# Kernel tuning notes

Hardware: AMD Instinct MI355X
Metric: run time of the kernel (lower is better)

The kernel has to match this reference:

```python
import jax, jax.numpy as jnp
import numpy as np

N, E, D = 10000, 160000, 512
H, C = 4, 128          # hidden layers: 4 heads x 128 = 512 (residual-compatible)
HF, CF = 2, 512        # final layer: 2 heads, concat=False (mean)
NEG_SLOPE = 0.2


def _gat(x, src, dst, W, a_src, a_dst, b, heads, out_c, concat):
    """PyG-style GATConv (v1 attention), no dropout (eval mode)."""
    n = x.shape[0]
    h = (x @ W).reshape(n, heads, out_c)                  # [N,H,C]
    es = (h * a_src).sum(-1)                              # [N,H]
    ed = (h * a_dst).sum(-1)                              # [N,H]
    e = jax.nn.leaky_relu(es[src] + ed[dst], NEG_SLOPE)   # [E,H]
    m = jax.ops.segment_max(e, dst, num_segments=n)       # softmax over in-edges of dst
    m = jnp.where(jnp.isfinite(m), m, 0.0)                # guard isolated nodes
    ex = jnp.exp(e - m[dst])
    den = jax.ops.segment_sum(ex, dst, num_segments=n)
    alpha = ex / (den[dst] + 1e-16)                       # [E,H]
    msg = h[src] * alpha[..., None]                       # [E,H,C]
    out = jax.ops.segment_sum(msg, dst, num_segments=n)   # [N,H,C]
    out = out.reshape(n, heads * out_c) if concat else out.mean(axis=1)
    return out + b


def setup_inputs() -> dict:
    key = jax.random.key(0)
    ks = jax.random.split(key, 16)
    s = 0.05
    return {
        "graph": jax.random.normal(ks[0], (N, D), jnp.float32),
        "edge_index": jax.random.randint(ks[1], (2, E), 0, N, dtype=jnp.int32),
        "W1": jax.random.normal(ks[2], (D, H * C), jnp.float32) * s,
        "as1": jax.random.normal(ks[3], (H, C), jnp.float32) * s,
        "ad1": jax.random.normal(ks[4], (H, C), jnp.float32) * s,
        "b1": jnp.zeros((H * C,), jnp.float32),
        "W2": jax.random.normal(ks[5], (H * C, H * C), jnp.float32) * s,
        "as2": jax.random.normal(ks[6], (H, C), jnp.float32) * s,
        "ad2": jax.random.normal(ks[7], (H, C), jnp.float32) * s,
        "b2": jnp.zeros((H * C,), jnp.float32),
        "W3": jax.random.normal(ks[8], (H * C, HF * CF), jnp.float32) * s,
        "as3": jax.random.normal(ks[9], (HF, CF), jnp.float32) * s,
        "ad3": jax.random.normal(ks[10], (HF, CF), jnp.float32) * s,
        "b3": jnp.zeros((CF,), jnp.float32),
    }


def reference(graph, edge_index, W1, as1, ad1, b1, W2, as2, ad2, b2, W3, as3, ad3, b3):
    src, dst = edge_index[0], edge_index[1]
    # layer_size=2: conv1 + convs[0] with ELU+residual, convs[1] (concat=False) residual only
    x = jax.nn.elu(_gat(graph, src, dst, W1, as1, ad1, b1, H, C, True) + graph)
    x = jax.nn.elu(_gat(x, src, dst, W2, as2, ad2, b2, H, C, True) + x)
    x = _gat(x, src, dst, W3, as3, ad3, b3, HF, CF, False) + x
    return x
```

## Files before the change

### kernel.cpp

```cpp
#include <hip/hip_runtime.h>
#include <hip/hip_bf16.h>
#include <hip/hip_fp16.h>
#include <cstddef>
#include <cstdint>


typedef _Float16 half8 __attribute__((ext_vector_type(8)));
typedef _Float16 half4v __attribute__((ext_vector_type(4)));
typedef _Float16 half2v __attribute__((ext_vector_type(2)));
typedef float floatx4 __attribute__((ext_vector_type(4)));

#define AS1(p) ((const __attribute__((address_space(1))) void*)(p))
#define AS3(p) ((__attribute__((address_space(3))) void*)(p))


__global__ void count_deg(const int* __restrict__ dst, int* __restrict__ deg, int E) {
    int e = blockIdx.x * blockDim.x + threadIdx.x;
    if (e < E) atomicAdd(&deg[dst[e]], 1);
}

__global__ void scan_kernel(const int* __restrict__ deg, int* __restrict__ row_start,
                            int* __restrict__ cursor, int n) {
    __shared__ int wsum[16];
    __shared__ int carry_s;
    int tid = threadIdx.x;
    int wave = tid >> 6, lane = tid & 63;
    if (tid == 0) { carry_s = 0; row_start[0] = 0; }
    __syncthreads();
    for (int base = 0; base < n; base += 1024) {
        int i = base + tid;
        int v = (i < n) ? deg[i] : 0;
        int x = v;
#pragma unroll
        for (int off = 1; off < 64; off <<= 1) {
            int t = __shfl_up(x, off);
            if (lane >= off) x += t;
        }
        if (lane == 63) wsum[wave] = x;
        __syncthreads();
        if (wave == 0 && lane < 16) {
            int w = wsum[lane];
#pragma unroll
            for (int off = 1; off < 16; off <<= 1) {
                int t = __shfl_up(w, off);
                if (lane >= off) w += t;
            }
            wsum[lane] = w;
        }
        __syncthreads();
        int carry = carry_s;
        int incl = x + (wave ? wsum[wave - 1] : 0) + carry;
        if (i < n) { row_start[i + 1] = incl; cursor[i] = incl - v; }
        __syncthreads();
        if (tid == 1023) carry_s = incl;
        __syncthreads();
    }
}

__global__ void scatter_edges(const int* __restrict__ src, const int* __restrict__ dst,
                              int* __restrict__ cursor, int* __restrict__ srcs, int E) {
    int e = blockIdx.x * blockDim.x + threadIdx.x;
    if (e < E) {
        int p = atomicAdd(&cursor[dst[e]], 1);
        srcs[p] = src[e];
    }
}


__global__ void cast_f16(const float* __restrict__ in, _Float16* __restrict__ out, int n4) {
    int i = blockIdx.x * blockDim.x + threadIdx.x;
    if (i < n4) {
        float4 v = ((const float4*)in)[i];
        half4v o = {(_Float16)v.x, (_Float16)v.y, (_Float16)v.z, (_Float16)v.w};
        ((half4v*)out)[i] = o;
    }
}

__global__ void transpose_cast_g(const float* __restrict__ in, _Float16* __restrict__ out,
                                 int in_ld, int out_ld) {
    __shared__ float t[32][33];
    int r0 = blockIdx.y * 32, c0 = blockIdx.x * 32;
    int tx = threadIdx.x, ty = threadIdx.y;
    for (int i = ty; i < 32; i += 8)
        t[i][tx] = in[(size_t)(r0 + i) * in_ld + c0 + tx];
    __syncthreads();
    for (int i = ty; i < 32; i += 8)
        out[(size_t)(c0 + i) * out_ld + r0 + tx] = (_Float16)t[tx][i];
}

__global__ void proj_all(const float* __restrict__ W1, const float* __restrict__ as1,
                         const float* __restrict__ ad1,
                         const float* __restrict__ W2, const float* __restrict__ as2,
                         const float* __restrict__ ad2,
                         const float* __restrict__ W3, const float* __restrict__ as3,
                         const float* __restrict__ ad3,
                         _Float16* __restrict__ Wt1, _Float16* __restrict__ Wt2,
                         float* __restrict__ wes3, float* __restrict__ wed3) {
    int w = (blockIdx.x * blockDim.x + threadIdx.x) >> 6;
    int lane = threadIdx.x & 63;
    if (w < 8192) {
        int layer = w >> 12;
        int idx = w & 4095;
        int d = idx & 511, hh = (idx >> 9) & 3, sel = idx >> 11;
        const float* W = layer ? W2 : W1;
        const float* a = layer ? (sel ? ad2 : as2) : (sel ? ad1 : as1);
        const float* row = W + (size_t)d * 512 + hh * 128;
        const float* av = a + hh * 128;
        float s = 0.f;
        s += row[lane] * av[lane];
        s += row[lane + 64] * av[lane + 64];
#pragma unroll
        for (int off = 32; off; off >>= 1) s += __shfl_down(s, off);
        if (lane == 0) {
            _Float16* Wt = layer ? Wt2 : Wt1;
            Wt[(size_t)(512 + sel * 4 + hh) * 512 + d] = (_Float16)s;
        }
    } else if (w < 10240) {
        int idx = w - 8192;
        int k = idx & 511, hh = (idx >> 9) & 1, sel = idx >> 10;
        const float* a = (sel ? ad3 : as3) + hh * 512;
        const float* row = W3 + (size_t)k * 1024 + hh * 512;
        float s = 0.f;
        for (int c = lane; c < 512; c += 64) s += row[c] * a[c];
#pragma unroll
        for (int off = 32; off; off >>= 1) s += __shfl_down(s, off);
        if (lane == 0) (sel ? wed3 : wes3)[hh * 512 + k] = s;
    } else if (w < 11136) {
        int z = (w - 10240) * 64 + lane;
        int layer = z / 28672;
        int rem = z - layer * 28672;
        int row = 520 + rem / 512, col = rem & 511;
        (layer ? Wt2 : Wt1)[(size_t)row * 512 + col] = (_Float16)0.f;
    }
}


#define BK 64

__global__ __launch_bounds__(256) void gemm_f16_att(const _Float16* __restrict__ A,
                                                    const _Float16* __restrict__ Bt,
                                                    _Float16* __restrict__ Hout,
                                                    float* __restrict__ es,
                                                    float* __restrict__ ed,
                                                    int M, int K) {
    __shared__ _Float16 As[64 * BK];
    __shared__ _Float16 Bs[64 * BK];
    int tid = threadIdx.x;
    int lane = tid & 63, wave = tid >> 6;
    int wm = (wave & 1) * 32, wn = (wave >> 1) * 32;
    int m0 = blockIdx.y * 64, n0 = blockIdx.x * 64;
    int l15 = lane & 15, quad = lane >> 4;
    int trow = tid >> 3, tcol = tid & 7;

    floatx4 acc[2][2];
#pragma unroll
    for (int i = 0; i < 2; ++i)
#pragma unroll
        for (int j = 0; j < 2; ++j) acc[i][j] = (floatx4){0.f, 0.f, 0.f, 0.f};

    for (int k0 = 0; k0 < K; k0 += BK) {
        __syncthreads();
#pragma unroll
        for (int i = 0; i < 2; ++i) {
            int gr = m0 + i * 32 + trow; if (gr >= M) gr = M - 1;
            __builtin_amdgcn_global_load_lds(AS1(A + (size_t)gr * K + k0 + tcol * 8),
                                             AS3(As + (size_t)(i * 256 + tid) * 8), 16, 0, 0);
        }
#pragma unroll
        for (int i = 0; i < 2; ++i) {
            int gr = n0 + i * 32 + trow;
            __builtin_amdgcn_global_load_lds(AS1(Bt + (size_t)gr * K + k0 + tcol * 8),
                                             AS3(Bs + (size_t)(i * 256 + tid) * 8), 16, 0, 0);
        }
        __syncthreads();
#pragma unroll
        for (int ks = 0; ks < BK; ks += 32) {
            half8 af[2], bfr[2];
#pragma unroll
            for (int i = 0; i < 2; ++i)
                af[i] = *(const half8*)&As[(wm + i * 16 + l15) * BK + ks + quad * 8];
#pragma unroll
            for (int j = 0; j < 2; ++j)
                bfr[j] = *(const half8*)&Bs[(wn + j * 16 + l15) * BK + ks + quad * 8];
#pragma unroll
            for (int i = 0; i < 2; ++i)
#pragma unroll
                for (int j = 0; j < 2; ++j)
                    acc[i][j] = __builtin_amdgcn_mfma_f32_16x16x32_f16(af[i], bfr[j], acc[i][j], 0, 0, 0);
        }
    }
#pragma unroll
    for (int i = 0; i < 2; ++i)
#pragma unroll
        for (int j = 0; j < 2; ++j) {
            int col = n0 + wn + j * 16 + l15;
#pragma unroll
            for (int r = 0; r < 4; ++r) {
                int row = m0 + wm + i * 16 + quad * 4 + r;
                if (row < M) {
                    float v = acc[i][j][r];
                    if (col < 512) Hout[(size_t)row * 512 + col] = (_Float16)v;
                    else if (col < 516) es[row * 4 + col - 512] = v;
                    else if (col < 520) ed[row * 4 + col - 516] = v;
                }
            }
        }
}

__global__ __launch_bounds__(256) void gemm_f16_ep(const _Float16* __restrict__ A,
                                                   const _Float16* __restrict__ Bt,
                                                   float* __restrict__ out,
                                                   const float* __restrict__ bias,
                                                   const _Float16* __restrict__ xres,
                                                   int M, int Nn, int K) {
    __shared__ _Float16 As[64 * BK];
    __shared__ _Float16 Bs[64 * BK];
    int tid = threadIdx.x;
    int lane = tid & 63, wave = tid >> 6;
    int wm = (wave & 1) * 32, wn = (wave >> 1) * 32;
    int m0 = blockIdx.y * 64, n0 = blockIdx.x * 64;
    int l15 = lane & 15, quad = lane >> 4;
    int trow = tid >> 3, tcol = tid & 7;

    floatx4 acc[2][2];
#pragma unroll
    for (int i = 0; i < 2; ++i)
#pragma unroll
        for (int j = 0; j < 2; ++j) acc[i][j] = (floatx4){0.f, 0.f, 0.f, 0.f};

    for (int k0 = 0; k0 < K; k0 += BK) {
        __syncthreads();
#pragma unroll
        for (int i = 0; i < 2; ++i) {
            int gr = m0 + i * 32 + trow; if (gr >= M) gr = M - 1;
            __builtin_amdgcn_global_load_lds(AS1(A + (size_t)gr * K + k0 + tcol * 8),
                                             AS3(As + (size_t)(i * 256 + tid) * 8), 16, 0, 0);
        }
#pragma unroll
        for (int i = 0; i < 2; ++i) {
            int gr = n0 + i * 32 + trow;
            __builtin_amdgcn_global_load_lds(AS1(Bt + (size_t)gr * K + k0 + tcol * 8),
                                             AS3(Bs + (size_t)(i * 256 + tid) * 8), 16, 0, 0);
        }
        __syncthreads();
#pragma unroll
        for (int ks = 0; ks < BK; ks += 32) {
            half8 af[2], bfr[2];
#pragma unroll
            for (int i = 0; i < 2; ++i)
                af[i] = *(const half8*)&As[(wm + i * 16 + l15) * BK + ks + quad * 8];
#pragma unroll
            for (int j = 0; j < 2; ++j)
                bfr[j] = *(const half8*)&Bs[(wn + j * 16 + l15) * BK + ks + quad * 8];
#pragma unroll
            for (int i = 0; i < 2; ++i)
#pragma unroll
                for (int j = 0; j < 2; ++j)
                    acc[i][j] = __builtin_amdgcn_mfma_f32_16x16x32_f16(af[i], bfr[j], acc[i][j], 0, 0, 0);
        }
    }
#pragma unroll
    for (int i = 0; i < 2; ++i)
#pragma unroll
        for (int j = 0; j < 2; ++j) {
            int col = n0 + wn + j * 16 + l15;
#pragma unroll
            for (int r = 0; r < 4; ++r) {
                int row = m0 + wm + i * 16 + quad * 4 + r;
                if (row < M)
                    out[(size_t)row * Nn + col] =
                        0.5f * acc[i][j][r] + bias[col] + (float)xres[(size_t)row * Nn + col];
            }
        }
}


template <int H>
__global__ __launch_bounds__(256) void attn_alpha2(
    const float* __restrict__ es, const float* __restrict__ ed,
    const int* __restrict__ row_start, const int* __restrict__ srcs,
    float* __restrict__ alpha, float* __restrict__ den, int Nn, int E) {
    const int EP = 64 / H;
    int wave = threadIdx.x >> 6, lane = threadIdx.x & 63;
    int n = blockIdx.x * 4 + wave;
    if (n >= Nn) return;
    int h = lane & (H - 1);
    int eslot = lane / H;
    float edn = ed[n * H + h];
    int beg = row_start[n], end = row_start[n + 1];
    float m = -INFINITY;
    for (int j0 = beg; j0 < end; j0 += EP) {
        int j = j0 + eslot;
        float e = -INFINITY;
        if (j < end) {
            e = es[srcs[j] * H + h] + edn;
            e = (e > 0.f) ? e : 0.2f * e;
            alpha[(size_t)h * E + j] = e;
        }
        m = fmaxf(m, e);
    }
#pragma unroll
    for (int off = H; off < 64; off <<= 1) m = fmaxf(m, __shfl_xor(m, off));
    float dsum = 0.f;
    for (int j0 = beg; j0 < end; j0 += EP) {
        int j = j0 + eslot;
        if (j < end) {
            float w = __expf(alpha[(size_t)h * E + j] - m);
            alpha[(size_t)h * E + j] = w;
            dsum += w;
        }
    }
#pragma unroll
    for (int off = H; off < 64; off <<= 1) dsum += __shfl_xor(dsum, off);
    if (lane < H) den[n * H + lane] = dsum;
}


template <bool RES32, bool COEF3>
__global__ __launch_bounds__(512) void aggregate4_concat(
    const _Float16* __restrict__ h, const float* __restrict__ alpha,
    const float* __restrict__ den,
    const int* __restrict__ row_start, const int* __restrict__ srcs,
    const float* __restrict__ bias, const float* __restrict__ xres32,
    const _Float16* __restrict__ xres16, _Float16* __restrict__ x_out_h,
    const float* __restrict__ wes3, const float* __restrict__ wed3,
    float* __restrict__ es3, float* __restrict__ ed3, int E) {
    __shared__ float red[8][512];
    __shared__ float csum[8][4];
    int n = blockIdx.x;
    int tid = threadIdx.x;
    int slot = tid >> 6, lane = tid & 63;
    int head = lane >> 4;
    int c0 = lane * 8;
    const float* al = alpha + (size_t)head * E;
    int beg = row_start[n], end = row_start[n + 1];
    float acc[8] = {};
    int j = beg + slot;
    for (; j + 8 < end; j += 16) {
        int s0 = srcs[j], s1 = srcs[j + 8];
        float w0 = al[j], w1 = al[j + 8];
        half8 h0 = *(const half8*)&h[(size_t)s0 * 512 + c0];
        half8 h1 = *(const half8*)&h[(size_t)s1 * 512 + c0];
#pragma unroll
        for (int k = 0; k < 8; ++k) acc[k] += w0 * (float)h0[k];
#pragma unroll
        for (int k = 0; k < 8; ++k) acc[k] += w1 * (float)h1[k];
    }
    if (j < end) {
        int s = srcs[j];
        float w = al[j];
        half8 hv = *(const half8*)&h[(size_t)s * 512 + c0];
#pragma unroll
        for (int k = 0; k < 8; ++k) acc[k] += w * (float)hv[k];
    }
#pragma unroll
    for (int k = 0; k < 8; ++k) red[slot][c0 + k] = acc[k];
    __syncthreads();
    int c = tid;
    float invden = 1.f / (den[n * 4 + (c >> 7)] + 1e-16f);
    float s = red[0][c] + red[1][c] + red[2][c] + red[3][c] +
              red[4][c] + red[5][c] + red[6][c] + red[7][c];
    size_t base = (size_t)n * 512 + c;
    float res = RES32 ? xres32[base] : (float)xres16[base];
    float v = s * invden + bias[c] + res;
    v = (v > 0.f) ? v : expm1f(v);
    x_out_h[base] = (_Float16)v;
    if (COEF3) {
        float t0 = v * wes3[c], t1 = v * wes3[512 + c];
        float t2 = v * wed3[c], t3 = v * wed3[512 + c];
#pragma unroll
        for (int off = 32; off; off >>= 1) {
            t0 += __shfl_down(t0, off);
            t1 += __shfl_down(t1, off);
            t2 += __shfl_down(t2, off);
            t3 += __shfl_down(t3, off);
        }
        if (lane == 0) {
            csum[slot][0] = t0; csum[slot][1] = t1;
            csum[slot][2] = t2; csum[slot][3] = t3;
        }
        __syncthreads();
        if (tid == 0) {
            float a0 = 0, a1 = 0, a2 = 0, a3 = 0;
#pragma unroll
            for (int w = 0; w < 8; ++w) {
                a0 += csum[w][0]; a1 += csum[w][1];
                a2 += csum[w][2]; a3 += csum[w][3];
            }
            es3[n * 2] = a0; es3[n * 2 + 1] = a1;
            ed3[n * 2] = a2; ed3[n * 2 + 1] = a3;
        }
    }
}


__global__ __launch_bounds__(512) void aggregate_x_dual(
    const _Float16* __restrict__ x, const float* __restrict__ alpha,
    const float* __restrict__ den,
    const int* __restrict__ row_start, const int* __restrict__ srcs,
    _Float16* __restrict__ y, int E) {
    __shared__ float red[8][1024];
    int n = blockIdx.x;
    int tid = threadIdx.x;
    int slot = tid >> 6, lane = tid & 63;
    int c0 = lane * 8;
    const float* al0 = alpha;
    const float* al1 = alpha + E;
    int beg = row_start[n], end = row_start[n + 1];
    float a0[8] = {}, a1[8] = {};
    int j = beg + slot;
    for (; j + 8 < end; j += 16) {
        int s0 = srcs[j], s1 = srcs[j + 8];
        float u0 = al0[j], v0 = al1[j];
        float u1 = al0[j + 8], v1 = al1[j + 8];
        half8 h0 = *(const half8*)&x[(size_t)s0 * 512 + c0];
        half8 h1 = *(const half8*)&x[(size_t)s1 * 512 + c0];
#pragma unroll
        for (int k = 0; k < 8; ++k) {
            float f = (float)h0[k];
            a0[k] += u0 * f;
            a1[k] += v0 * f;
        }
#pragma unroll
        for (int k = 0; k < 8; ++k) {
            float f = (float)h1[k];
            a0[k] += u1 * f;
            a1[k] += v1 * f;
        }
    }
    if (j < end) {
        int s = srcs[j];
        float u = al0[j], v = al1[j];
        half8 hv = *(const half8*)&x[(size_t)s * 512 + c0];
#pragma unroll
        for (int k = 0; k < 8; ++k) {
            float f = (float)hv[k];
            a0[k] += u * f;
            a1[k] += v * f;
        }
    }
#pragma unroll
    for (int k = 0; k < 8; ++k) {
        red[slot][c0 + k] = a0[k];
        red[slot][512 + c0 + k] = a1[k];
    }
    __syncthreads();
    float invd0 = 1.f / (den[n * 2] + 1e-16f);
    float invd1 = 1.f / (den[n * 2 + 1] + 1e-16f);
    int c = tid * 2;
    float inv = (c < 512) ? invd0 : invd1;
    half2v o;
#pragma unroll
    for (int k = 0; k < 2; ++k) {
        float s = red[0][c + k] + red[1][c + k] + red[2][c + k] + red[3][c + k] +
                  red[4][c + k] + red[5][c + k] + red[6][c + k] + red[7][c + k];
        o[k] = (_Float16)(s * inv);
    }
    *(half2v*)&y[(size_t)n * 1024 + c] = o;
}


extern "C" void kernel_launch(void* const* d_in, const int* in_sizes, int n_in,
                              void* d_out, int out_size, void* d_ws, size_t ws_size,
                              hipStream_t stream) {
    const float* graph = (const float*)d_in[0];
    const int* edge_index = (const int*)d_in[1];
    const float* W1 = (const float*)d_in[2];
    const float* as1 = (const float*)d_in[3];
    const float* ad1 = (const float*)d_in[4];
    const float* b1 = (const float*)d_in[5];
    const float* W2 = (const float*)d_in[6];
    const float* as2 = (const float*)d_in[7];
    const float* ad2 = (const float*)d_in[8];
    const float* b2 = (const float*)d_in[9];
    const float* W3 = (const float*)d_in[10];
    const float* as3 = (const float*)d_in[11];
    const float* ad3 = (const float*)d_in[12];
    const float* b3 = (const float*)d_in[13];

    const int D = 512;
    int N = in_sizes[0] / D;
    int E = in_sizes[1] / 2;
    const int* src = edge_index;
    const int* dst = edge_index + E;

    char* p = (char*)d_ws;
    auto carve = [&](size_t bytes) {
        void* r = (void*)p;
        p += (bytes + 255) & ~(size_t)255;
        return r;
    };
    _Float16* Ah   = (_Float16*)carve((size_t)N * 512 * 2);
    _Float16* Wt1  = (_Float16*)carve((size_t)576 * 512 * 2);
    _Float16* Wt2  = (_Float16*)carve((size_t)576 * 512 * 2);
    _Float16* Bt3  = (_Float16*)carve((size_t)512 * 1024 * 2);
    _Float16* h_h  = (_Float16*)carve((size_t)N * 1024 * 2);
    float* es      = (float*)carve((size_t)N * 4 * 4);
    float* ed      = (float*)carve((size_t)N * 4 * 4);
    float* den     = (float*)carve((size_t)N * 4 * 4);
    float* alpha   = (float*)carve((size_t)4 * E * 4);
    float* wes3    = (float*)carve((size_t)2 * 512 * 4);
    float* wed3    = (float*)carve((size_t)2 * 512 * 4);
    int* deg       = (int*)carve((size_t)N * 4);
    int* cur       = (int*)carve((size_t)N * 4);
    int* row_st    = (int*)carve((size_t)(N + 1) * 4);
    int* srcs      = (int*)carve((size_t)E * 4);

    hipMemsetAsync(deg, 0, (size_t)N * 4, stream);
    count_deg<<<(E + 255) / 256, 256, 0, stream>>>(dst, deg, E);
    scan_kernel<<<1, 1024, 0, stream>>>(deg, row_st, cur, N);
    scatter_edges<<<(E + 255) / 256, 256, 0, stream>>>(src, dst, cur, srcs, E);

    cast_f16<<<(N * 512 / 4 + 255) / 256, 256, 0, stream>>>(graph, Ah, N * 512 / 4);
    dim3 tblk(32, 8);
    transpose_cast_g<<<dim3(16, 16), tblk, 0, stream>>>(W1, Wt1, 512, 512);
    transpose_cast_g<<<dim3(16, 16), tblk, 0, stream>>>(W2, Wt2, 512, 512);
    transpose_cast_g<<<dim3(16, 16), tblk, 0, stream>>>(W3, Bt3, 1024, 1024);
    transpose_cast_g<<<dim3(16, 16), tblk, 0, stream>>>(W3 + 512, Bt3 + 512, 1024, 1024);
    proj_all<<<2784, 256, 0, stream>>>(W1, as1, ad1, W2, as2, ad2, W3, as3, ad3,
                                       Wt1, Wt2, wes3, wed3);

    int nblk4 = (N + 3) / 4;
    int mblk = (N + 63) / 64;
    gemm_f16_att<<<dim3(9, mblk), 256, 0, stream>>>(Ah, Wt1, h_h, es, ed, N, 512);
    attn_alpha2<4><<<nblk4, 256, 0, stream>>>(es, ed, row_st, srcs, alpha, den, N, E);
    aggregate4_concat<true, false><<<N, 512, 0, stream>>>(
        h_h, alpha, den, row_st, srcs, b1, graph, nullptr, Ah,
        nullptr, nullptr, nullptr, nullptr, E);

    gemm_f16_att<<<dim3(9, mblk), 256, 0, stream>>>(Ah, Wt2, h_h, es, ed, N, 512);
    attn_alpha2<4><<<nblk4, 256, 0, stream>>>(es, ed, row_st, srcs, alpha, den, N, E);
    aggregate4_concat<false, true><<<N, 512, 0, stream>>>(
        h_h, alpha, den, row_st, srcs, b2, nullptr, Ah, Ah,
        wes3, wed3, es, ed, E);

    attn_alpha2<2><<<nblk4, 256, 0, stream>>>(es, ed, row_st, srcs, alpha, den, N, E);
    aggregate_x_dual<<<N, 512, 0, stream>>>(Ah, alpha, den, row_st, srcs, h_h, E);
    gemm_f16_ep<<<dim3(8, mblk), 256, 0, stream>>>(
        h_h, Bt3, (float*)d_out, b3, Ah, N, 512, 1024);
}
```

Measured before the change: 337.3 us.

## Map one wavefront per node in GAT aggregation kernels, dropping LDS reduction

The three neighbour-aggregation kernels used to give each node a 512-thread block whose eight waves split that node's in-edges, then combined the partial sums through shared memory with barriers. They now assign one 64-lane wave per node and pack eight nodes per block. Each wave walks the node's whole edge list and writes the epilogue directly with 8-wide vector stores. The layer-3 coefficient dot product is reduced with wave shuffles only. This removes LDS traffic, barriers and the cross-wave reduction. In exchange, each node's edges are processed serially within one wave, which shortens available memory-level parallelism per node and can cause load imbalance on high-degree nodes.

New measurement: 339.9 us. About the same (+0.8%).

```diff
diff --git a/kernel.cpp b/kernel.cpp
--- a/kernel.cpp
+++ b/kernel.cpp
@@ -317,28 +317,26 @@
 
 
 template <bool RES32, bool COEF3>
-__global__ __launch_bounds__(512) void aggregate4_concat(
+__global__ __launch_bounds__(512) void aggregate5_concat(
     const _Float16* __restrict__ h, const float* __restrict__ alpha,
     const float* __restrict__ den,
     const int* __restrict__ row_start, const int* __restrict__ srcs,
     const float* __restrict__ bias, const float* __restrict__ xres32,
     const _Float16* __restrict__ xres16, _Float16* __restrict__ x_out_h,
     const float* __restrict__ wes3, const float* __restrict__ wed3,
-    float* __restrict__ es3, float* __restrict__ ed3, int E) {
-    __shared__ float red[8][512];
-    __shared__ float csum[8][4];
-    int n = blockIdx.x;
-    int tid = threadIdx.x;
-    int slot = tid >> 6, lane = tid & 63;
+    float* __restrict__ es3, float* __restrict__ ed3, int Nn, int E) {
+    int wave = threadIdx.x >> 6, lane = threadIdx.x & 63;
+    int n = blockIdx.x * 8 + wave;
+    if (n >= Nn) return;
     int head = lane >> 4;
     int c0 = lane * 8;
     const float* al = alpha + (size_t)head * E;
     int beg = row_start[n], end = row_start[n + 1];
     float acc[8] = {};
-    int j = beg + slot;
-    for (; j + 8 < end; j += 16) {
-        int s0 = srcs[j], s1 = srcs[j + 8];
-        float w0 = al[j], w1 = al[j + 8];
+    int j = beg;
+    for (; j + 1 < end; j += 2) {
+        int s0 = srcs[j], s1 = srcs[j + 1];
+        float w0 = al[j], w1 = al[j + 1];
         half8 h0 = *(const half8*)&h[(size_t)s0 * 512 + c0];
         half8 h1 = *(const half8*)&h[(size_t)s1 * 512 + c0];
 #pragma unroll
@@ -353,21 +351,28 @@
 #pragma unroll
         for (int k = 0; k < 8; ++k) acc[k] += w * (float)hv[k];
     }
-#pragma unroll
-    for (int k = 0; k < 8; ++k) red[slot][c0 + k] = acc[k];
-    __syncthreads();
-    int c = tid;
-    float invden = 1.f / (den[n * 4 + (c >> 7)] + 1e-16f);
-    float s = red[0][c] + red[1][c] + red[2][c] + red[3][c] +
-              red[4][c] + red[5][c] + red[6][c] + red[7][c];
-    size_t base = (size_t)n * 512 + c;
-    float res = RES32 ? xres32[base] : (float)xres16[base];
-    float v = s * invden + bias[c] + res;
-    v = (v > 0.f) ? v : expm1f(v);
-    x_out_h[base] = (_Float16)v;
+    float invden = 1.f / (den[n * 4 + head] + 1e-16f);
+    size_t base = (size_t)n * 512 + c0;
+    float v[8];
+    half8 o;
+#pragma unroll
+    for (int k = 0; k < 8; ++k) {
+        float res = RES32 ? xres32[base + k] : (float)xres16[base + k];
+        float t = acc[k] * invden + bias[c0 + k] + res;
+        t = (t > 0.f) ? t : expm1f(t);
+        v[k] = t;
+        o[k] = (_Float16)t;
+    }
+    *(half8*)&x_out_h[base] = o;
     if (COEF3) {
-        float t0 = v * wes3[c], t1 = v * wes3[512 + c];
-        float t2 = v * wed3[c], t3 = v * wed3[512 + c];
+        float t0 = 0.f, t1 = 0.f, t2 = 0.f, t3 = 0.f;
+#pragma unroll
+        for (int k = 0; k < 8; ++k) {
+            t0 += v[k] * wes3[c0 + k];
+            t1 += v[k] * wes3[512 + c0 + k];
+            t2 += v[k] * wed3[c0 + k];
+            t3 += v[k] * wed3[512 + c0 + k];
+        }
 #pragma unroll
         for (int off = 32; off; off >>= 1) {
             t0 += __shfl_down(t0, off);
@@ -376,43 +381,31 @@
             t3 += __shfl_down(t3, off);
         }
         if (lane == 0) {
-            csum[slot][0] = t0; csum[slot][1] = t1;
-            csum[slot][2] = t2; csum[slot][3] = t3;
-        }
-        __syncthreads();
-        if (tid == 0) {
-            float a0 = 0, a1 = 0, a2 = 0, a3 = 0;
-#pragma unroll
-            for (int w = 0; w < 8; ++w) {
-                a0 += csum[w][0]; a1 += csum[w][1];
-                a2 += csum[w][2]; a3 += csum[w][3];
-            }
-            es3[n * 2] = a0; es3[n * 2 + 1] = a1;
-            ed3[n * 2] = a2; ed3[n * 2 + 1] = a3;
-        }
-    }
-}
-
-
-__global__ __launch_bounds__(512) void aggregate_x_dual(
+            es3[n * 2] = t0; es3[n * 2 + 1] = t1;
+            ed3[n * 2] = t2; ed3[n * 2 + 1] = t3;
+        }
+    }
+}
+
+
+__global__ __launch_bounds__(512) void aggregate5_dual(
     const _Float16* __restrict__ x, const float* __restrict__ alpha,
     const float* __restrict__ den,
     const int* __restrict__ row_start, const int* __restrict__ srcs,
-    _Float16* __restrict__ y, int E) {
-    __shared__ float red[8][1024];
-    int n = blockIdx.x;
-    int tid = threadIdx.x;
-    int slot = tid >> 6, lane = tid & 63;
+    _Float16* __restrict__ y, int Nn, int E) {
+    int wave = threadIdx.x >> 6, lane = threadIdx.x & 63;
+    int n = blockIdx.x * 8 + wave;
+    if (n >= Nn) return;
     int c0 = lane * 8;
     const float* al0 = alpha;
     const float* al1 = alpha + E;
     int beg = row_start[n], end = row_start[n + 1];
     float a0[8] = {}, a1[8] = {};
-    int j = beg + slot;
-    for (; j + 8 < end; j += 16) {
-        int s0 = srcs[j], s1 = srcs[j + 8];
+    int j = beg;
+    for (; j + 1 < end; j += 2) {
+        int s0 = srcs[j], s1 = srcs[j + 1];
         float u0 = al0[j], v0 = al1[j];
-        float u1 = al0[j + 8], v1 = al1[j + 8];
+        float u1 = al0[j + 1], v1 = al1[j + 1];
         half8 h0 = *(const half8*)&x[(size_t)s0 * 512 + c0];
         half8 h1 = *(const half8*)&x[(size_t)s1 * 512 + c0];
 #pragma unroll
@@ -439,24 +432,16 @@
             a1[k] += v * f;
         }
     }
-#pragma unroll
-    for (int k = 0; k < 8; ++k) {
-        red[slot][c0 + k] = a0[k];
-        red[slot][512 + c0 + k] = a1[k];
-    }
-    __syncthreads();
     float invd0 = 1.f / (den[n * 2] + 1e-16f);
     float invd1 = 1.f / (den[n * 2 + 1] + 1e-16f);
-    int c = tid * 2;
-    float inv = (c < 512) ? invd0 : invd1;
-    half2v o;
-#pragma unroll
-    for (int k = 0; k < 2; ++k) {
-        float s = red[0][c + k] + red[1][c + k] + red[2][c + k] + red[3][c + k] +
-                  red[4][c + k] + red[5][c + k] + red[6][c + k] + red[7][c + k];
-        o[k] = (_Float16)(s * inv);
-    }
-    *(half2v*)&y[(size_t)n * 1024 + c] = o;
+    half8 o0, o1;
+#pragma unroll
+    for (int k = 0; k < 8; ++k) {
+        o0[k] = (_Float16)(a0[k] * invd0);
+        o1[k] = (_Float16)(a1[k] * invd1);
+    }
+    *(half8*)&y[(size_t)n * 1024 + c0] = o0;
+    *(half8*)&y[(size_t)n * 1024 + 512 + c0] = o1;
 }
 
 
@@ -521,21 +506,22 @@
                                        Wt1, Wt2, wes3, wed3);
 
     int nblk4 = (N + 3) / 4;
+    int nblk8 = (N + 7) / 8;
     int mblk = (N + 63) / 64;
     gemm_f16_att<<<dim3(9, mblk), 256, 0, stream>>>(Ah, Wt1, h_h, es, ed, N, 512);
     attn_alpha2<4><<<nblk4, 256, 0, stream>>>(es, ed, row_st, srcs, alpha, den, N, E);
-    aggregate4_concat<true, false><<<N, 512, 0, stream>>>(
+    aggregate5_concat<true, false><<<nblk8, 512, 0, stream>>>(
         h_h, alpha, den, row_st, srcs, b1, graph, nullptr, Ah,
-        nullptr, nullptr, nullptr, nullptr, E);
+        nullptr, nullptr, nullptr, nullptr, N, E);
 
     gemm_f16_att<<<dim3(9, mblk), 256, 0, stream>>>(Ah, Wt2, h_h, es, ed, N, 512);
     attn_alpha2<4><<<nblk4, 256, 0, stream>>>(es, ed, row_st, srcs, alpha, den, N, E);
-    aggregate4_concat<false, true><<<N, 512, 0, stream>>>(
+    aggregate5_concat<false, true><<<nblk8, 512, 0, stream>>>(
         h_h, alpha, den, row_st, srcs, b2, nullptr, Ah, Ah,
-        wes3, wed3, es, ed, E);
+        wes3, wed3, es, ed, N, E);
 
     attn_alpha2<2><<<nblk4, 256, 0, stream>>>(es, ed, row_st, srcs, alpha, den, N, E);
-    aggregate_x_dual<<<N, 512, 0, stream>>>(Ah, alpha, den, row_st, srcs, h_h, E);
+    aggregate5_dual<<<nblk8, 512, 0, stream>>>(Ah, alpha, den, row_st, srcs, h_h, N, E);
     gemm_f16_ep<<<dim3(8, mblk), 256, 0, stream>>>(
         h_h, Bt3, (float*)d_out, b3, Ah, N, 512, 1024);
 }
```
